# Kernel optimization log

Hardware: AMD Instinct MI355X
Metric: run time of the kernel (lower is better)

The kernel has to match this reference:

```python
import jax, jax.numpy as jnp
import numpy as np
from jax import lax

DIM = 256
SFEAT = 8
N_ITER = 2
EPS_LN = 1e-6


def unfold_patches(x):
    """x: (..., H, W) -> (..., 9, H, W); patch k=(ki*3+kj) is x shifted by (ki-1, kj-1),
    matching conv2d with eye(9) kernel and padding=1."""
    H, W = x.shape[-2], x.shape[-1]
    pad = [(0, 0)] * (x.ndim - 2) + [(1, 1), (1, 1)]
    xp = jnp.pad(x, pad)
    return jnp.stack([xp[..., i:i + H, j:j + W] for i in range(3) for j in range(3)], axis=-3)


def fold_patches(y):
    """y: (..., 9, H, W) -> (..., H, W); adjoint of unfold_patches (conv_transpose2d with eye kernel)."""
    H, W = y.shape[-2], y.shape[-1]
    pad = [(0, 0)] * (y.ndim - 2) + [(1, 1), (1, 1)]
    yp = jnp.pad(y, pad)
    out = jnp.zeros(y.shape[:-3] + (H, W), y.dtype)
    for k in range(9):
        ki, kj = divmod(k, 3)
        out = out + yp[..., k, 2 - ki:2 - ki + H, 2 - kj:2 - kj + W]
    return out


def depthwise_conv(x, w, b, pad):
    # x: (B,C,H,W), w: (C,1,k,k)
    y = lax.conv_general_dilated(x, w, (1, 1), [(pad, pad), (pad, pad)],
                                 feature_group_count=x.shape[1],
                                 dimension_numbers=('NCHW', 'OIHW', 'NCHW'))
    return y + b[None, :, None, None]


def conv1x1(x, w, b):
    # w: (Cout, Cin)
    return jnp.einsum('bchw,oc->bohw', x, w) + b[None, :, None, None]


def layernorm2d(x, w, b):
    mu = x.mean(axis=1, keepdims=True)
    var = ((x - mu) ** 2).mean(axis=1, keepdims=True)
    xn = (x - mu) / jnp.sqrt(var + EPS_LN)
    return xn * w[None, :, None, None] + b[None, :, None, None]


def sfg_forward(x, r1_w, r1_b, rd_w, rd_b, r2_w, r2_b):
    B, C, H, W = x.shape
    h = w = SFEAT
    hh, ww = H // h, W // w
    N = hh * ww
    scale = C ** (-0.5)

    x6 = x.reshape(B, C, hh, h, ww, w)
    stokens = x6.mean(axis=(3, 5))                                  # (B,C,hh,ww) adaptive avg pool
    pf = x6.transpose(0, 2, 4, 3, 5, 1).reshape(B, N, h * w, C)     # (B,N,hw,C)

    aff = None
    asum = None
    for it in range(N_ITER):
        patches = unfold_patches(stokens)                           # (B,C,9,hh,ww)
        patches = patches.transpose(0, 3, 4, 1, 2).reshape(B, N, C, 9)
        aff = jax.nn.softmax(jnp.einsum('bnpc,bnck->bnpk', pf, patches) * scale, axis=-1)
        asum = fold_patches(aff.sum(axis=2).transpose(0, 2, 1).reshape(B, 9, hh, ww))
        asum = asum[:, None]                                        # (B,1,hh,ww)
        if it < N_ITER - 1:
            st = jnp.einsum('bnpc,bnpk->bnck', pf, aff).reshape(B * C, 9, hh, ww)
            st = fold_patches(st).reshape(B, C, hh, ww)
            stokens = st / (asum + 1e-12)

    st = jnp.einsum('bnpc,bnpk->bnck', pf, aff).reshape(B * C, 9, hh, ww)
    stokens = fold_patches(st).reshape(B, C, hh, ww) / (lax.stop_gradient(asum) + 1e-12)

    # refine: 1x1 -> depthwise 5x5 -> 1x1
    stokens = conv1x1(stokens, r1_w, r1_b)
    stokens = depthwise_conv(stokens, rd_w, rd_b, pad=2)
    stokens = conv1x1(stokens, r2_w, r2_b)

    sp = unfold_patches(stokens).transpose(0, 3, 4, 1, 2).reshape(B, N, C, 9)
    po = jnp.einsum('bnck,bnpk->bncp', sp, aff)                     # (B,N,C,hw)
    po = po.reshape(B, hh, ww, C, h, w).transpose(0, 3, 1, 4, 2, 5).reshape(B, C, H, W)
    return po


def setup_inputs() -> dict:
    key = jax.random.key(0)
    ks = jax.random.split(key, 12)
    B, C, H, W = 4, DIM, 256, 256
    f32 = jnp.float32
    return {
        'x': jax.random.normal(ks[0], (B, C, H, W), f32),
        'dwc_w': jax.random.normal(ks[1], (C, 1, 3, 3), f32) * 0.1,
        'dwc_b': jnp.zeros((C,), f32),
        'ln_w': jnp.ones((C,), f32),
        'ln_b': jnp.zeros((C,), f32),
        'r1_w': jax.random.normal(ks[2], (C, C), f32) * (C ** -0.5),
        'r1_b': jnp.zeros((C,), f32),
        'rd_w': jax.random.normal(ks[3], (C, 1, 5, 5), f32) * 0.1,
        'rd_b': jnp.zeros((C,), f32),
        'r2_w': jax.random.normal(ks[4], (C, C), f32) * (C ** -0.5),
        'r2_b': jnp.zeros((C,), f32),
        'gamma': 1e-5 * jnp.ones((1, C, 1, 1), f32),
    }


def reference(x, dwc_w, dwc_b, ln_w, ln_b, r1_w, r1_b, rd_w, rd_b, r2_w, r2_b, gamma):
    # pos_embed: x + DWC(x)
    x = x + depthwise_conv(x, dwc_w, dwc_b, pad=1)
    residual = gamma * sfg_forward(layernorm2d(x, ln_w, ln_b), r1_w, r1_b, rd_w, rd_b, r2_w, r2_b)
    return x + residual
```

## Files before the change

### kernel.cpp

```cpp
#include <hip/hip_runtime.h>
#include <hip/hip_bf16.h>

#define NPB 1024
#define EPS_LN 1e-6f

__global__ __launch_bounds__(256) void k_dwc_ln(
        const float* __restrict__ x, const float* __restrict__ dwc_w,
        const float* __restrict__ dwc_b, float* __restrict__ x1,
        float* __restrict__ part1, float* __restrict__ part2)
{
    const int b = blockIdx.z;
    const int cg = blockIdx.y;
    const int w = threadIdx.x >> 6;
    const int lane = threadIdx.x & 63;
    const int y = blockIdx.x * 4 + w;
    const int x0 = lane << 2;
    const int c0 = cg * 64;
    const float* xb = x + (((size_t)(b * 256 + c0)) << 16);
    float* x1b = x1 + (((size_t)(b * 256 + c0)) << 16);
    const float4 z4 = {0.f, 0.f, 0.f, 0.f};
    float4 s1v = z4, s2v = z4;
    for (int ci = 0; ci < 64; ++ci) {
        const float* xc = xb + ((size_t)ci << 16);
        const float* wp = dwc_w + (size_t)(c0 + ci) * 9;
        const float w00 = wp[0], w01 = wp[1], w02 = wp[2];
        const float w10 = wp[3], w11 = wp[4], w12 = wp[5];
        const float w20 = wp[6], w21 = wp[7], w22 = wp[8];
        const float bb = dwc_b[c0 + ci];
        float4 r0 = (y > 0)   ? *(const float4*)(xc + (((y - 1) << 8) + x0)) : z4;
        float4 r1 =             *(const float4*)(xc + ((y << 8) + x0));
        float4 r2 = (y < 255) ? *(const float4*)(xc + (((y + 1) << 8) + x0)) : z4;
        float L0 = __shfl_up(r0.w, 1), L1 = __shfl_up(r1.w, 1), L2 = __shfl_up(r2.w, 1);
        float R0 = __shfl_down(r0.x, 1), R1 = __shfl_down(r1.x, 1), R2 = __shfl_down(r2.x, 1);
        if (lane == 0)  { L0 = 0.f; L1 = 0.f; L2 = 0.f; }
        if (lane == 63) { R0 = 0.f; R1 = 0.f; R2 = 0.f; }
        float4 acc;
        acc.x = bb + w00 * L0   + w01 * r0.x + w02 * r0.y
                   + w10 * L1   + w11 * r1.x + w12 * r1.y
                   + w20 * L2   + w21 * r2.x + w22 * r2.y;
        acc.y = bb + w00 * r0.x + w01 * r0.y + w02 * r0.z
                   + w10 * r1.x + w11 * r1.y + w12 * r1.z
                   + w20 * r2.x + w21 * r2.y + w22 * r2.z;
        acc.z = bb + w00 * r0.y + w01 * r0.z + w02 * r0.w
                   + w10 * r1.y + w11 * r1.z + w12 * r1.w
                   + w20 * r2.y + w21 * r2.z + w22 * r2.w;
        acc.w = bb + w00 * r0.z + w01 * r0.w + w02 * R0
                   + w10 * r1.z + w11 * r1.w + w12 * R1
                   + w20 * r2.z + w21 * r2.w + w22 * R2;
        float4 v1;
        v1.x = r1.x + acc.x; v1.y = r1.y + acc.y;
        v1.z = r1.z + acc.z; v1.w = r1.w + acc.w;
        *(float4*)(x1b + (((size_t)ci << 16) + (y << 8) + x0)) = v1;
        s1v.x += v1.x; s1v.y += v1.y; s1v.z += v1.z; s1v.w += v1.w;
        s2v.x += v1.x * v1.x; s2v.y += v1.y * v1.y;
        s2v.z += v1.z * v1.z; s2v.w += v1.w * v1.w;
    }
    const size_t po = (((size_t)(cg * 4 + b)) << 16) + (y << 8) + x0;
    *(float4*)(part1 + po) = s1v;
    *(float4*)(part2 + po) = s2v;
}

__global__ __launch_bounds__(256) void k_ln_fin(
        const float* __restrict__ part1, const float* __restrict__ part2,
        float* __restrict__ meanb, float* __restrict__ rstdb)
{
    const int b = blockIdx.y, y = blockIdx.x, xx = threadIdx.x;
    const int off = (y << 8) + xx;
    float s1 = 0.f, s2 = 0.f;
    #pragma unroll
    for (int cg = 0; cg < 4; ++cg) {
        size_t p = (((size_t)(cg * 4 + b)) << 16) + off;
        s1 += part1[p]; s2 += part2[p];
    }
    float mu = s1 * (1.f / 256.f);
    float var = s2 * (1.f / 256.f) - mu * mu;
    meanb[((size_t)b << 16) + off] = mu;
    rstdb[((size_t)b << 16) + off] = rsqrtf(var + EPS_LN);
}

__global__ __launch_bounds__(256) void k_stokens0(
        const float* __restrict__ x1, const float* __restrict__ meanb,
        const float* __restrict__ rstdb, const float* __restrict__ lnw,
        const float* __restrict__ lnb, float* __restrict__ stA)
{
    const int c = blockIdx.x, b = blockIdx.y;
    const int tx = threadIdx.x;
    const float w = lnw[c], bb = lnb[c];
    const float* xp = x1 + ((size_t)(b * 256 + c) << 16);
    const float* mp = meanb + ((size_t)b << 16);
    const float* rp = rstdb + ((size_t)b << 16);
    for (int i = 0; i < 32; ++i) {
        float acc = 0.f;
        for (int dy = 0; dy < 8; ++dy) {
            int y = i * 8 + dy;
            float v = xp[(y << 8) + tx];
            acc += (v - mp[(y << 8) + tx]) * rp[(y << 8) + tx] * w + bb;
        }
        acc += __shfl_xor(acc, 1);
        acc += __shfl_xor(acc, 2);
        acc += __shfl_xor(acc, 4);
        if ((tx & 7) == 0) {
            int j = tx >> 3;
            stA[(((size_t)b * NPB + i * 32 + j) << 8) + c] = acc * (1.f / 64.f);
        }
    }
}

template <int ITER>
__global__ __launch_bounds__(256) void k_aff(
        const float* __restrict__ x1, const float* __restrict__ meanb,
        const float* __restrict__ rstdb, const float* __restrict__ lnw,
        const float* __restrict__ lnb, const float* __restrict__ stok_in,
        const float* __restrict__ asum_in, float* __restrict__ stok_out,
        float* __restrict__ asum_out, __hip_bfloat16* __restrict__ aff_out)
{
    __shared__ __hip_bfloat16 pf[256][66];
    __shared__ float pat[256][12];
    __shared__ float sa[64][12];
    __shared__ float mu_s[64], rs_s[64];
    __shared__ float lnw_s[256], lnb_s[256];

    const int blk = blockIdx.x;
    const int b = blk >> 10, n = blk & 1023;
    const int pi = n >> 5, pj = n & 31;
    const int tid = threadIdx.x;

    lnw_s[tid] = lnw[tid];
    lnb_s[tid] = lnb[tid];
    if (tid < 64) {
        int py = tid >> 3, px = tid & 7;
        size_t off = ((size_t)b << 16) + ((pi * 8 + py) << 8) + pj * 8 + px;
        mu_s[tid] = meanb[off];
        rs_s[tid] = rstdb[off];
    }
    {
        int c = tid;
        const float* sp = stok_in + (((size_t)b * NPB) << 8) + c;
        for (int k = 0; k < 9; ++k) {
            int ni = pi + k / 3 - 1, nj = pj + k % 3 - 1;
            float v = 0.f;
            if ((unsigned)ni < 32u && (unsigned)nj < 32u) {
                int nn = ni * 32 + nj;
                v = sp[(size_t)nn << 8];
                if (ITER == 1) v /= (asum_in[b * NPB + nn] + 1e-12f);
            }
            pat[c][k] = v;
        }
    }
    __syncthreads();
    {
        int c0 = tid >> 6, p = tid & 63;
        int py = p >> 3, px = p & 7;
        const float mu = mu_s[p], rs = rs_s[p];
        const size_t base = ((size_t)b * 256) << 16;
        const int goff = ((pi * 8 + py) << 8) + pj * 8 + px;
        for (int cb = 0; cb < 64; ++cb) {
            int c = cb * 4 + c0;
            float v = x1[base + ((size_t)c << 16) + goff];
            float xl = (v - mu) * rs * lnw_s[c] + lnb_s[c];
            pf[c][p] = __float2bfloat16(xl);
        }
    }
    __syncthreads();
    for (int o = tid; o < 576; o += 256) {
        int p = o / 9, k = o - (o / 9) * 9;
        float s = 0.f;
        for (int c = 0; c < 256; ++c)
            s += __bfloat162float(pf[c][p]) * pat[c][k];
        sa[p][k] = s * 0.0625f;
    }
    __syncthreads();
    if (tid < 64) {
        int p = tid;
        float m = sa[p][0];
        for (int k = 1; k < 9; ++k) m = fmaxf(m, sa[p][k]);
        float e[9], sum = 0.f;
        for (int k = 0; k < 9; ++k) { e[k] = __expf(sa[p][k] - m); sum += e[k]; }
        float inv = 1.f / sum;
        for (int k = 0; k < 9; ++k) sa[p][k] = e[k] * inv;
    }
    __syncthreads();
    if (ITER == 1) {
        for (int o = tid; o < 576; o += 256)
            aff_out[(size_t)blk * 576 + o] = __float2bfloat16(sa[o / 9][o % 9]);
    }
    if (tid < 9) {
        float s = 0.f;
        for (int p = 0; p < 64; ++p) s += sa[p][tid];
        int ni = pi + tid / 3 - 1, nj = pj + tid % 3 - 1;
        if ((unsigned)ni < 32u && (unsigned)nj < 32u)
            atomicAdd(&asum_out[b * NPB + ni * 32 + nj], s);
    }
    {
        int c = tid;
        float acc[9];
        for (int k = 0; k < 9; ++k) acc[k] = 0.f;
        for (int p = 0; p < 64; ++p) {
            float v = __bfloat162float(pf[c][p]);
            for (int k = 0; k < 9; ++k) acc[k] += v * sa[p][k];
        }
        for (int k = 0; k < 9; ++k) {
            int ni = pi + k / 3 - 1, nj = pj + k % 3 - 1;
            if ((unsigned)ni < 32u && (unsigned)nj < 32u)
                atomicAdd(&stok_out[(((size_t)b * NPB + ni * 32 + nj) << 8) + c], acc[k]);
        }
    }
}

template <int NORM>
__global__ __launch_bounds__(256) void k_conv1x1(
        const float* __restrict__ in, const float* __restrict__ asum,
        const float* __restrict__ w, const float* __restrict__ bias,
        float* __restrict__ out)
{
    __shared__ float in_s[8][256];
    const int pix0 = blockIdx.x * 8;
    const int tid = threadIdx.x;
    for (int p = 0; p < 8; ++p) {
        int gp = pix0 + p;
        float v = in[((size_t)gp << 8) + tid];
        if (NORM) v /= (asum[gp] + 1e-12f);
        in_s[p][tid] = v;
    }
    __syncthreads();
    const int o = tid;
    float bb = bias[o];
    float acc[8];
    for (int p = 0; p < 8; ++p) acc[p] = bb;
    const float4* w4 = (const float4*)(w + (size_t)o * 256);
    for (int c4 = 0; c4 < 64; ++c4) {
        float4 wv = w4[c4];
        for (int p = 0; p < 8; ++p) {
            acc[p] += in_s[p][c4 * 4 + 0] * wv.x + in_s[p][c4 * 4 + 1] * wv.y
                    + in_s[p][c4 * 4 + 2] * wv.z + in_s[p][c4 * 4 + 3] * wv.w;
        }
    }
    for (int p = 0; p < 8; ++p)
        out[((size_t)(pix0 + p) << 8) + o] = acc[p];
}

__global__ __launch_bounds__(256) void k_dwc5(
        const float* __restrict__ in, const float* __restrict__ w,
        const float* __restrict__ bias, float* __restrict__ out)
{
    const int i = blockIdx.x, b = blockIdx.y;
    const int c = threadIdx.x;
    float wr[25];
    for (int t = 0; t < 25; ++t) wr[t] = w[c * 25 + t];
    const float bb = bias[c];
    const float* inb = in + (((size_t)b * NPB) << 8) + c;
    float* outb = out + (((size_t)b * NPB) << 8) + c;
    for (int j = 0; j < 32; ++j) {
        float acc = bb;
        for (int di = 0; di < 5; ++di) {
            int y = i + di - 2;
            if ((unsigned)y >= 32u) continue;
            for (int dj = 0; dj < 5; ++dj) {
                int xv = j + dj - 2;
                if ((unsigned)xv >= 32u) continue;
                acc += inb[(size_t)(y * 32 + xv) << 8] * wr[di * 5 + dj];
            }
        }
        outb[(size_t)(i * 32 + j) << 8] = acc;
    }
}

__global__ __launch_bounds__(256) void k_final(
        const float* __restrict__ st3, const __hip_bfloat16* __restrict__ aff,
        const float* __restrict__ gamma, float* __restrict__ io)
{
    __shared__ float sp[256][12];
    __shared__ float af[64][12];
    const int blk = blockIdx.x;
    const int b = blk >> 10, n = blk & 1023;
    const int pi = n >> 5, pj = n & 31;
    const int tid = threadIdx.x;
    {
        int c = tid;
        const float* s0 = st3 + (((size_t)b * NPB) << 8) + c;
        for (int k = 0; k < 9; ++k) {
            int ni = pi + k / 3 - 1, nj = pj + k % 3 - 1;
            float v = 0.f;
            if ((unsigned)ni < 32u && (unsigned)nj < 32u)
                v = s0[(size_t)(ni * 32 + nj) << 8];
            sp[c][k] = v;
        }
    }
    for (int o = tid; o < 576; o += 256)
        af[o / 9][o % 9] = __bfloat162float(aff[(size_t)blk * 576 + o]);
    __syncthreads();
    const int cq = tid >> 4;
    const int p4 = tid & 15;
    const int py = p4 >> 1, px0 = (p4 & 1) * 4;
    float afr[4][9];
    #pragma unroll
    for (int j = 0; j < 4; ++j)
        #pragma unroll
        for (int k = 0; k < 9; ++k) afr[j][k] = af[p4 * 4 + j][k];
    const int gy = pi * 8 + py, gx = pj * 8 + px0;
    const size_t base = (((size_t)b * 256) << 16) + (gy << 8) + gx;
    for (int pass = 0; pass < 16; ++pass) {
        const int c = pass * 16 + cq;
        const float g = gamma[c];
        float s[9];
        #pragma unroll
        for (int k = 0; k < 9; ++k) s[k] = sp[c][k];
        float4 po = {0.f, 0.f, 0.f, 0.f};
        #pragma unroll
        for (int k = 0; k < 9; ++k) {
            po.x += s[k] * afr[0][k]; po.y += s[k] * afr[1][k];
            po.z += s[k] * afr[2][k]; po.w += s[k] * afr[3][k];
        }
        float4* ptr = (float4*)(io + base + ((size_t)c << 16));
        float4 v = *ptr;
        v.x += g * po.x; v.y += g * po.y; v.z += g * po.z; v.w += g * po.w;
        *ptr = v;
    }
}

extern "C" void kernel_launch(void* const* d_in, const int* in_sizes, int n_in,
                              void* d_out, int out_size, void* d_ws, size_t ws_size,
                              hipStream_t stream)
{
    (void)in_sizes; (void)n_in; (void)out_size; (void)ws_size;
    const float* x     = (const float*)d_in[0];
    const float* dwc_w = (const float*)d_in[1];
    const float* dwc_b = (const float*)d_in[2];
    const float* ln_w  = (const float*)d_in[3];
    const float* ln_b  = (const float*)d_in[4];
    const float* r1_w  = (const float*)d_in[5];
    const float* r1_b  = (const float*)d_in[6];
    const float* rd_w  = (const float*)d_in[7];
    const float* rd_b  = (const float*)d_in[8];
    const float* r2_w  = (const float*)d_in[9];
    const float* r2_b  = (const float*)d_in[10];
    const float* gamma = (const float*)d_in[11];
    float* out = (float*)d_out;
    float* ws  = (float*)d_ws;

    float* stA   = ws;
    float* stB   = ws + 1048576;
    float* stC   = ws + 2097152;
    float* asum0 = ws + 3145728;
    float* asum1 = ws + 3149824;
    float* meanb = ws + 3153920;
    float* rstdb = ws + 3416064;
    __hip_bfloat16* affb = (__hip_bfloat16*)(ws + 3678208);
    float* part1 = ws + 4857856;
    float* part2 = ws + 5906432;

    hipMemsetAsync(stB, 0, (size_t)(2 * 1048576 + 2 * 4096) * sizeof(float), stream);

    k_dwc_ln<<<dim3(64, 4, 4), 256, 0, stream>>>(x, dwc_w, dwc_b, out, part1, part2);
    k_ln_fin<<<dim3(256, 4), 256, 0, stream>>>(part1, part2, meanb, rstdb);
    k_stokens0<<<dim3(256, 4), 256, 0, stream>>>(out, meanb, rstdb, ln_w, ln_b, stA);
    k_aff<0><<<4096, 256, 0, stream>>>(out, meanb, rstdb, ln_w, ln_b,
                                       stA, nullptr, stB, asum0, nullptr);
    k_aff<1><<<4096, 256, 0, stream>>>(out, meanb, rstdb, ln_w, ln_b,
                                       stB, asum0, stC, asum1, affb);
    k_conv1x1<1><<<512, 256, 0, stream>>>(stC, asum1, r1_w, r1_b, stA);
    k_dwc5<<<dim3(32, 4), 256, 0, stream>>>(stA, rd_w, rd_b, stB);
    k_conv1x1<0><<<512, 256, 0, stream>>>(stB, nullptr, r2_w, r2_b, stC);
    k_final<<<4096, 256, 0, stream>>>(stC, affb, gamma, out);
}
```

Measured before the change: 1.444 ms.

## Retile final residual kernel to process full image rows per block

The final kernel changes from one block per 8x8 superpixel patch (all 256 channels) to one block per patch-row across 64 channels, with 512 threads. Each block stages a 3x34x64 halo of superpixel features in shared memory and has each warp read and write contiguous full 256-wide image rows. The aim is more coalesced float4 read-modify-write traffic on the large output tensor than the old scattered 8-wide patch accesses gave. In exchange there are fewer blocks and the affinity values are read directly from global memory in strided bf16 loads.

```diff
diff --git a/kernel.cpp b/kernel.cpp
--- a/kernel.cpp
+++ b/kernel.cpp
@@ -265,53 +265,64 @@
     }
 }
 
-__global__ __launch_bounds__(256) void k_final(
+__global__ __launch_bounds__(512) void k_final(
         const float* __restrict__ st3, const __hip_bfloat16* __restrict__ aff,
         const float* __restrict__ gamma, float* __restrict__ io)
 {
-    __shared__ float sp[256][12];
-    __shared__ float af[64][12];
-    const int blk = blockIdx.x;
-    const int b = blk >> 10, n = blk & 1023;
-    const int pi = n >> 5, pj = n & 31;
+    __shared__ float sp_s[3][34][66];
+    const int pi = blockIdx.x;
+    const int cg = blockIdx.y;
+    const int b  = blockIdx.z;
+    const int c0 = cg * 64;
     const int tid = threadIdx.x;
-    {
-        int c = tid;
-        const float* s0 = st3 + (((size_t)b * NPB) << 8) + c;
-        for (int k = 0; k < 9; ++k) {
-            int ni = pi + k / 3 - 1, nj = pj + k % 3 - 1;
-            float v = 0.f;
-            if ((unsigned)ni < 32u && (unsigned)nj < 32u)
-                v = s0[(size_t)(ni * 32 + nj) << 8];
-            sp[c][k] = v;
-        }
-    }
-    for (int o = tid; o < 576; o += 256)
-        af[o / 9][o % 9] = __bfloat162float(aff[(size_t)blk * 576 + o]);
-    __syncthreads();
-    const int cq = tid >> 4;
-    const int p4 = tid & 15;
-    const int py = p4 >> 1, px0 = (p4 & 1) * 4;
+
+    for (int t = tid; t < 3 * 34 * 64; t += 512) {
+        const int c  = t & 63;
+        const int rj = t >> 6;
+        const int jj = rj % 34;
+        const int r  = rj / 34;
+        const int nc = jj - 1;
+        const int nr = pi - 1 + r;
+        float v = 0.f;
+        if ((unsigned)nr < 32u && (unsigned)nc < 32u)
+            v = st3[(((size_t)(b * NPB + nr * 32 + nc)) << 8) + c0 + c];
+        sp_s[r][jj][c] = v;
+    }
+
+    const int y    = tid >> 6;
+    const int lane = tid & 63;
+    const int x0   = lane << 2;
+    const int pj   = x0 >> 3;
+    const int p0   = y * 8 + (x0 & 7);
+    const __hip_bfloat16* ab =
+        aff + ((size_t)(b * NPB + pi * 32 + pj)) * 576 + p0 * 9;
     float afr[4][9];
     #pragma unroll
     for (int j = 0; j < 4; ++j)
         #pragma unroll
-        for (int k = 0; k < 9; ++k) afr[j][k] = af[p4 * 4 + j][k];
-    const int gy = pi * 8 + py, gx = pj * 8 + px0;
-    const size_t base = (((size_t)b * 256) << 16) + (gy << 8) + gx;
-    for (int pass = 0; pass < 16; ++pass) {
-        const int c = pass * 16 + cq;
-        const float g = gamma[c];
-        float s[9];
+        for (int k = 0; k < 9; ++k)
+            afr[j][k] = __bfloat162float(ab[j * 9 + k]);
+
+    __syncthreads();
+
+    const size_t iobase = (((size_t)(b * 256 + c0)) << 16)
+                        + ((pi * 8 + y) << 8) + x0;
+    #pragma unroll 2
+    for (int ci = 0; ci < 64; ++ci) {
+        const float g = gamma[c0 + ci];
+        float spv[9];
         #pragma unroll
-        for (int k = 0; k < 9; ++k) s[k] = sp[c][k];
+        for (int kr = 0; kr < 3; ++kr)
+            #pragma unroll
+            for (int kc = 0; kc < 3; ++kc)
+                spv[kr * 3 + kc] = sp_s[kr][pj + kc][ci];
         float4 po = {0.f, 0.f, 0.f, 0.f};
         #pragma unroll
         for (int k = 0; k < 9; ++k) {
-            po.x += s[k] * afr[0][k]; po.y += s[k] * afr[1][k];
-            po.z += s[k] * afr[2][k]; po.w += s[k] * afr[3][k];
-        }
-        float4* ptr = (float4*)(io + base + ((size_t)c << 16));
+            po.x += spv[k] * afr[0][k]; po.y += spv[k] * afr[1][k];
+            po.z += spv[k] * afr[2][k]; po.w += spv[k] * afr[3][k];
+        }
+        float4* ptr = (float4*)(io + iobase + ((size_t)ci << 16));
         float4 v = *ptr;
         v.x += g * po.x; v.y += g * po.y; v.z += g * po.z; v.w += g * po.w;
         *ptr = v;
@@ -361,5 +372,5 @@
     k_conv1x1<1><<<512, 256, 0, stream>>>(stC, asum1, r1_w, r1_b, stA);
     k_dwc5<<<dim3(32, 4), 256, 0, stream>>>(stA, rd_w, rd_b, stB);
     k_conv1x1<0><<<512, 256, 0, stream>>>(stB, nullptr, r2_w, r2_b, stC);
-    k_final<<<4096, 256, 0, stream>>>(stC, affb, gamma, out);
-}
+    k_final<<<dim3(32, 4, 4), 512, 0, stream>>>(stC, affb, gamma, out);
+}
```

Measured after the change: 1.225 ms. 1.18x faster.
